# Kernel optimization log

Hardware: AMD Instinct MI355X
Metric: run time of the kernel (lower is better)

## Reference

```python
import jax, jax.numpy as jnp
import numpy as np

HEADS = 12
DIM_HEAD = 64
SCALE = DIM_HEAD ** -0.5

def setup_inputs() -> dict:
    key = jax.random.key(0)
    k1, k2, k3, k4 = jax.random.split(key, 4)
    dim, inner = 768, HEADS * DIM_HEAD
    x = jax.random.normal(k1, (4, 2048, dim), dtype=jnp.float32)
    w_qkv = jax.random.normal(k2, (dim, 3 * inner), dtype=jnp.float32) * (dim ** -0.5)
    w_out = jax.random.normal(k3, (inner, dim), dtype=jnp.float32) * (inner ** -0.5)
    b_out = jax.random.normal(k4, (dim,), dtype=jnp.float32) * 0.02
    return {"x": x, "w_qkv": w_qkv, "w_out": w_out, "b_out": b_out}

def reference(x, w_qkv, w_out, b_out):
    B, N, _ = x.shape
    qkv = jnp.einsum('bnd,de->bne', x, w_qkv)  # [B,N,3*inner]
    q, k, v = jnp.split(qkv, 3, axis=-1)
    # b n (h d) -> b h n d
    split_heads = lambda t: t.reshape(B, N, HEADS, DIM_HEAD).transpose(0, 2, 1, 3)
    q, k, v = split_heads(q), split_heads(k), split_heads(v)
    dots = jnp.einsum('bhnd,bhmd->bhnm', q, k) * SCALE  # [B,H,N,N]
    attn = jax.nn.softmax(dots, axis=-1)
    out = jnp.einsum('bhnm,bhmd->bhnd', attn, v)
    out = out.transpose(0, 2, 1, 3).reshape(B, N, HEADS * DIM_HEAD)  # b h n d -> b n (h d)
    return jnp.einsum('bne,ed->bnd', out, w_out) + b_out
```

## Files before the change

### kernel.cpp

```cpp
#include <hip/hip_runtime.h>
#include <stdint.h>

typedef unsigned short ushort_t;
typedef __attribute__((ext_vector_type(8))) short short8;
typedef __attribute__((ext_vector_type(4))) float f32x4;
typedef __attribute__((ext_vector_type(2))) uint32_t u32x2;

#define BATCH 4
#define SEQ 2048
#define DMODEL 768
#define NH 12
#define HD 64
#define QKV3 2304
#define NHEADS 48
#define SCALE_Q 0.18033688011112042f

__device__ __forceinline__ ushort_t f2bf(float f) {
    union { float f; uint32_t u; } v; v.f = f;
    uint32_t u = v.u;
    u += 0x7FFF + ((u >> 16) & 1);
    return (ushort_t)(u >> 16);
}

__device__ __forceinline__ uint32_t pack_bf16(float a, float b) {
#if __has_builtin(__builtin_amdgcn_cvt_pk_bf16_f32)
    typedef __attribute__((ext_vector_type(2))) __bf16 bf16x2;
    bf16x2 r = __builtin_amdgcn_cvt_pk_bf16_f32(a, b);
    return __builtin_bit_cast(uint32_t, r);
#else
    return ((uint32_t)f2bf(b) << 16) | (uint32_t)f2bf(a);
#endif
}

typedef __attribute__((address_space(1))) uint32_t as1_u32;
typedef __attribute__((address_space(3))) uint32_t as3_u32;
__device__ __forceinline__ void async16(void* lds, const void* gsrc) {
    __builtin_amdgcn_global_load_lds((as1_u32*)gsrc, (as3_u32*)lds, 16, 0, 0);
}

__device__ __forceinline__ void wait_vm_lgkm0() {
    __builtin_amdgcn_s_waitcnt(0x0070);
}
__device__ __forceinline__ void wait_vm4_lgkm0() {
    __builtin_amdgcn_s_waitcnt(0x0074);
}

__device__ __forceinline__ void swap32(uint32_t& a, uint32_t& b) {
    asm("v_permlane32_swap_b32 %0, %1" : "+v"(a), "+v"(b));
}
__device__ __forceinline__ void swap16(uint32_t& a, uint32_t& b) {
    asm("v_permlane16_swap_b32 %0, %1" : "+v"(a), "+v"(b));
}

__global__ __launch_bounds__(256) void cvt_bf16(
    const float* __restrict__ in, ushort_t* __restrict__ out) {
    int i = blockIdx.x * 256 + threadIdx.x;
    float4 v = *(const float4*)(in + (size_t)i * 4);
    ushort4 o; o.x = f2bf(v.x); o.y = f2bf(v.y); o.z = f2bf(v.z); o.w = f2bf(v.w);
    *(ushort4*)(out + (size_t)i * 4) = o;
}

__global__ __launch_bounds__(256) void transpose_f32_bf16(
    const float* __restrict__ in, ushort_t* __restrict__ out, int R, int C) {
    __shared__ ushort_t t[64][72];
    const int tid = threadIdx.x;
    const int r0 = blockIdx.y * 64, c0 = blockIdx.x * 64;
#pragma unroll
    for (int i = 0; i < 4; i++) {
        int idx = tid + i * 256;
        int row = idx >> 4, c4 = (idx & 15) * 4;
        float4 v = *(const float4*)(in + (size_t)(r0 + row) * C + c0 + c4);
        ushort4 o; o.x = f2bf(v.x); o.y = f2bf(v.y); o.z = f2bf(v.z); o.w = f2bf(v.w);
        *(ushort4*)&t[row][c4] = o;
    }
    __syncthreads();
#pragma unroll
    for (int i = 0; i < 2; i++) {
        int idx = tid + i * 256;
        int oc = idx >> 3, g8 = (idx & 7) * 8;
        ushort_t tmp[8];
#pragma unroll
        for (int e = 0; e < 8; e++) tmp[e] = t[g8 + e][oc];
        *(short8*)(out + (size_t)(c0 + oc) * R + r0 + g8) = *(const short8*)tmp;
    }
}

__global__ __launch_bounds__(256, 2) void gemm_qkv(
    const ushort_t* __restrict__ A, const ushort_t* __restrict__ B,
    ushort_t* __restrict__ qkv, ushort_t* __restrict__ vT) {
    __shared__ ushort_t As[2][128 * 64];
    __shared__ ushort_t Bs[2][128 * 64];

    const int tid = threadIdx.x;
    const int m0 = blockIdx.y * 128, n0 = blockIdx.x * 128;
    const int lane = tid & 63, w = tid >> 6;
    const int wm = w >> 1, wn = w & 1;
    const int l16 = lane & 15, quad = lane >> 4;

    f32x4 acc[4][4];
#pragma unroll
    for (int i = 0; i < 4; i++)
#pragma unroll
        for (int j = 0; j < 4; j++) acc[i][j] = (f32x4){0.f, 0.f, 0.f, 0.f};

    int srow[4], scol[4];
#pragma unroll
    for (int j = 0; j < 4; j++) {
        int s = j * 256 + tid;
        srow[j] = s >> 3;
        scol[j] = ((s & 7) ^ (srow[j] & 7)) * 8;
    }
    const int swz0 = (quad ^ (l16 & 7)) * 8;
    const int swz1 = ((4 + quad) ^ (l16 & 7)) * 8;

    auto stage = [&](int kt, int buf) {
#pragma unroll
        for (int j = 0; j < 4; j++) {
            async16(&As[buf][(j * 256 + w * 64) * 8],
                    A + (size_t)(m0 + srow[j]) * DMODEL + kt * 64 + scol[j]);
            async16(&Bs[buf][(j * 256 + w * 64) * 8],
                    B + (size_t)(n0 + srow[j]) * DMODEL + kt * 64 + scol[j]);
        }
    };

    stage(0, 0);
    const int NKT = DMODEL / 64;
    for (int t = 0; t < NKT; t++) {
        wait_vm_lgkm0();
        __builtin_amdgcn_s_barrier();
        if (t + 1 < NKT) stage(t + 1, (t + 1) & 1);

        const ushort_t* Asb = As[t & 1];
        const ushort_t* Bsb = Bs[t & 1];
        short8 a[4][2], b[4][2];
#pragma unroll
        for (int mi = 0; mi < 4; mi++) {
            int r = (wm * 64 + mi * 16 + l16) * 64;
            a[mi][0] = *(const short8*)&Asb[r + swz0];
            a[mi][1] = *(const short8*)&Asb[r + swz1];
        }
#pragma unroll
        for (int ni = 0; ni < 4; ni++) {
            int r = (wn * 64 + ni * 16 + l16) * 64;
            b[ni][0] = *(const short8*)&Bsb[r + swz0];
            b[ni][1] = *(const short8*)&Bsb[r + swz1];
        }
#pragma unroll
        for (int kk = 0; kk < 2; kk++)
#pragma unroll
            for (int mi = 0; mi < 4; mi++)
#pragma unroll
                for (int ni = 0; ni < 4; ni++)
                    acc[mi][ni] = __builtin_amdgcn_mfma_f32_16x16x32_bf16(
                        a[mi][kk], b[ni][kk], acc[mi][ni], 0, 0, 0);
    }

#pragma unroll
    for (int ni = 0; ni < 4; ni++) {
        int nbase = n0 + wn * 64 + ni * 16;
        int which = nbase / DMODEL;
        int rem = nbase - which * DMODEL;
        int h = rem >> 6;
        int d = (rem & 63) + l16;
        if (which == 2) {
#pragma unroll
            for (int mi = 0; mi < 4; mi++) {
                int mg = m0 + wm * 64 + mi * 16 + quad * 4;
                int b_ = mg >> 11, ns = mg & 2047;
                u32x2 pk = {pack_bf16(acc[mi][ni][0], acc[mi][ni][1]),
                            pack_bf16(acc[mi][ni][2], acc[mi][ni][3])};
                *(u32x2*)(vT + ((size_t)(b_ * NH + h) * HD + d) * SEQ + ns) = pk;
            }
        } else {
            float scale = (which == 0) ? SCALE_Q : 1.0f;
#pragma unroll
            for (int mi = 0; mi < 4; mi++) {
#pragma unroll
                for (int r = 0; r < 4; r++) {
                    int mg = m0 + wm * 64 + mi * 16 + quad * 4 + r;
                    int b_ = mg >> 11, ns = mg & 2047;
                    size_t dst = (((size_t)(which * BATCH + b_) * NH + h) * SEQ + ns) * HD + d;
                    qkv[dst] = f2bf(acc[mi][ni][r] * scale);
                }
            }
        }
    }
}

__global__ __launch_bounds__(256, 3) void attn(
    const ushort_t* __restrict__ qkv, const ushort_t* __restrict__ vT,
    ushort_t* __restrict__ ao) {
    __shared__ ushort_t smem[24576];

    const int tid = threadIdx.x;
    const int bid = blockIdx.x;
    const int i = bid >> 3;
    const int bh = (bid & 7) + 8 * (i % 6);
    const int qt = i / 6;
    const int lane = tid & 63, w = tid >> 6;
    const int l16 = lane & 15, quad = lane >> 4;
    const int qh7 = l16 & 7;

    const ushort_t* qh = qkv + (size_t)bh * (SEQ * HD);
    const ushort_t* kh = qkv + (size_t)(NHEADS + bh) * (SEQ * HD);
    const ushort_t* vh = vT + (size_t)bh * (HD * SEQ);

    short8 aq[2][2];
#pragma unroll
    for (int mi = 0; mi < 2; mi++)
#pragma unroll
        for (int kk = 0; kk < 2; kk++) {
            int row = qt * 128 + w * 32 + mi * 16 + l16;
            aq[mi][kk] = *(const short8*)(qh + (size_t)row * HD + kk * 32 + quad * 8);
        }

    short8 ones8;
#pragma unroll
    for (int j = 0; j < 8; j++) ones8[j] = (short)0x3F80;

    f32x4 acc_l[2];
    f32x4 O[4][2];
#pragma unroll
    for (int mi = 0; mi < 2; mi++) acc_l[mi] = (f32x4){0.f, 0.f, 0.f, 0.f};
#pragma unroll
    for (int nd = 0; nd < 4; nd++)
#pragma unroll
        for (int mi = 0; mi < 2; mi++) O[nd][mi] = (f32x4){0.f, 0.f, 0.f, 0.f};

    int srow[2], scol[2];
#pragma unroll
    for (int j = 0; j < 2; j++) {
        int s = j * 256 + tid;
        srow[j] = s >> 3;
        scol[j] = ((s & 7) ^ (srow[j] & 7)) * 8;
    }
    const int swz0 = (quad ^ qh7) * 8;
    const int swz1 = ((4 + quad) ^ qh7) * 8;

    auto stage = [&](int t, int buf) {
        int nb = buf * 8192, j1 = t * 64;
#pragma unroll
        for (int j = 0; j < 2; j++) {
            async16(&smem[nb + (j * 256 + w * 64) * 8],
                    kh + (size_t)(j1 + srow[j]) * HD + scol[j]);
            async16(&smem[nb + 4096 + (j * 256 + w * 64) * 8],
                    vh + (size_t)srow[j] * SEQ + j1 + scol[j]);
        }
    };

    auto compute = [&](const ushort_t* Ks) {
        const ushort_t* Vs = Ks + 4096;
#pragma unroll
        for (int p = 0; p < 2; p++) {
            uint32_t pkv[2][2][2];
#pragma unroll
            for (int sub = 0; sub < 2; sub++) {
                const int ni = p * 2 + sub;
                int r = (ni * 16 + l16) * 64;
                short8 ak0 = *(const short8*)&Ks[r + swz0];
                short8 ak1 = *(const short8*)&Ks[r + swz1];
#pragma unroll
                for (int mi = 0; mi < 2; mi++) {
                    f32x4 s = __builtin_amdgcn_mfma_f32_16x16x32_bf16(
                        ak0, aq[mi][0], (f32x4){0.f, 0.f, 0.f, 0.f}, 0, 0, 0);
                    s = __builtin_amdgcn_mfma_f32_16x16x32_bf16(
                        ak1, aq[mi][1], s, 0, 0, 0);
                    f32x4 pr;
#pragma unroll
                    for (int rr = 0; rr < 4; rr++)
                        pr[rr] = __builtin_amdgcn_exp2f(s[rr]);
                    pkv[sub][mi][0] = pack_bf16(pr[0], pr[1]);
                    pkv[sub][mi][1] = pack_bf16(pr[2], pr[3]);
                }
            }
            short8 bp32[2];
#pragma unroll
            for (int mi = 0; mi < 2; mi++) {
                uint32_t x0 = pkv[0][mi][0], y0 = pkv[1][mi][0];
                uint32_t x1 = pkv[0][mi][1], y1 = pkv[1][mi][1];
                swap32(x0, y0); swap16(x0, y0);
                swap32(x1, y1); swap16(x1, y1);
                union { short8 s; uint32_t u[4]; } bu;
                bu.u[0] = x0; bu.u[1] = x1; bu.u[2] = y0; bu.u[3] = y1;
                bp32[mi] = bu.s;
            }
            __builtin_amdgcn_s_setprio(1);
#pragma unroll
            for (int mi = 0; mi < 2; mi++)
                acc_l[mi] = __builtin_amdgcn_mfma_f32_16x16x32_bf16(
                    ones8, bp32[mi], acc_l[mi], 0, 0, 0);
#pragma unroll
            for (int nd = 0; nd < 4; nd++) {
                int vrow = nd * 16 + l16;
                short8 av = *(const short8*)&Vs[vrow * 64 +
                                                (((p * 4 + quad) ^ qh7) * 8)];
#pragma unroll
                for (int mi = 0; mi < 2; mi++)
                    O[nd][mi] = __builtin_amdgcn_mfma_f32_16x16x32_bf16(
                        av, bp32[mi], O[nd][mi], 0, 0, 0);
            }
            __builtin_amdgcn_s_setprio(0);
        }
    };

    stage(0, 0);
    stage(1, 1);

    const int NT = SEQ / 64;
    for (int t = 0; t < NT - 1; t++) {
        wait_vm4_lgkm0();
        __builtin_amdgcn_s_barrier();
        if (t + 2 < NT) stage(t + 2, (t + 2) % 3);
        compute(smem + (t % 3) * 8192);
    }
    wait_vm_lgkm0();
    __builtin_amdgcn_s_barrier();
    compute(smem + ((NT - 1) % 3) * 8192);

    float inv[2];
#pragma unroll
    for (int mi = 0; mi < 2; mi++)
        inv[mi] = __builtin_amdgcn_rcpf(acc_l[mi][0]);
    __syncthreads();
    ushort_t* Lt = smem;
#pragma unroll
    for (int mi = 0; mi < 2; mi++)
#pragma unroll
        for (int nd = 0; nd < 4; nd++) {
            int row = w * 32 + mi * 16 + l16;
            int col = nd * 16 + quad * 4;
            uint32_t d0 = pack_bf16(O[nd][mi][0] * inv[mi], O[nd][mi][1] * inv[mi]);
            uint32_t d1 = pack_bf16(O[nd][mi][2] * inv[mi], O[nd][mi][3] * inv[mi]);
            *(u32x2*)&Lt[row * 72 + col] = (u32x2){d0, d1};
        }
    __syncthreads();

    const int b_ = bh / NH, h = bh % NH;
#pragma unroll
    for (int i2 = 0; i2 < 4; i2++) {
        int idx = tid + i2 * 256;
        int row = idx >> 3, c8 = (idx & 7) * 8;
        short8 vv = *(const short8*)&Lt[row * 72 + c8];
        *(short8*)(ao + ((size_t)(b_ * SEQ + qt * 128 + row)) * DMODEL +
                   h * HD + c8) = vv;
    }
}

__global__ __launch_bounds__(256, 2) void gemm_out(
    const ushort_t* __restrict__ A, const ushort_t* __restrict__ B,
    const float* __restrict__ bias, float* __restrict__ out) {
    __shared__ ushort_t As[2][128 * 64];
    __shared__ ushort_t Bs[2][128 * 64];

    const int tid = threadIdx.x;
    const int m0 = blockIdx.y * 128, n0 = blockIdx.x * 128;
    const int lane = tid & 63, w = tid >> 6;
    const int wm = w >> 1, wn = w & 1;
    const int l16 = lane & 15, quad = lane >> 4;

    f32x4 acc[4][4];
#pragma unroll
    for (int i = 0; i < 4; i++)
#pragma unroll
        for (int j = 0; j < 4; j++) acc[i][j] = (f32x4){0.f, 0.f, 0.f, 0.f};

    int srow[4], scol[4];
#pragma unroll
    for (int j = 0; j < 4; j++) {
        int s = j * 256 + tid;
        srow[j] = s >> 3;
        scol[j] = ((s & 7) ^ (srow[j] & 7)) * 8;
    }
    const int swz0 = (quad ^ (l16 & 7)) * 8;
    const int swz1 = ((4 + quad) ^ (l16 & 7)) * 8;

    auto stage = [&](int kt, int buf) {
#pragma unroll
        for (int j = 0; j < 4; j++) {
            async16(&As[buf][(j * 256 + w * 64) * 8],
                    A + (size_t)(m0 + srow[j]) * DMODEL + kt * 64 + scol[j]);
            async16(&Bs[buf][(j * 256 + w * 64) * 8],
                    B + (size_t)(n0 + srow[j]) * DMODEL + kt * 64 + scol[j]);
        }
    };

    stage(0, 0);
    const int NKT = DMODEL / 64;
    for (int t = 0; t < NKT; t++) {
        wait_vm_lgkm0();
        __builtin_amdgcn_s_barrier();
        if (t + 1 < NKT) stage(t + 1, (t + 1) & 1);

        const ushort_t* Asb = As[t & 1];
        const ushort_t* Bsb = Bs[t & 1];
        short8 a[4][2], b[4][2];
#pragma unroll
        for (int mi = 0; mi < 4; mi++) {
            int r = (wm * 64 + mi * 16 + l16) * 64;
            a[mi][0] = *(const short8*)&Asb[r + swz0];
            a[mi][1] = *(const short8*)&Asb[r + swz1];
        }
#pragma unroll
        for (int ni = 0; ni < 4; ni++) {
            int r = (wn * 64 + ni * 16 + l16) * 64;
            b[ni][0] = *(const short8*)&Bsb[r + swz0];
            b[ni][1] = *(const short8*)&Bsb[r + swz1];
        }
#pragma unroll
        for (int kk = 0; kk < 2; kk++)
#pragma unroll
            for (int mi = 0; mi < 4; mi++)
#pragma unroll
                for (int ni = 0; ni < 4; ni++)
                    acc[mi][ni] = __builtin_amdgcn_mfma_f32_16x16x32_bf16(
                        a[mi][kk], b[ni][kk], acc[mi][ni], 0, 0, 0);
    }

#pragma unroll
    for (int ni = 0; ni < 4; ni++) {
        int ng = n0 + wn * 64 + ni * 16 + l16;
        float bv = bias[ng];
#pragma unroll
        for (int mi = 0; mi < 4; mi++) {
#pragma unroll
            for (int r = 0; r < 4; r++) {
                int mg = m0 + wm * 64 + mi * 16 + quad * 4 + r;
                out[(size_t)mg * DMODEL + ng] = acc[mi][ni][r] + bv;
            }
        }
    }
}

extern "C" void kernel_launch(void* const* d_in, const int* in_sizes, int n_in,
                              void* d_out, int out_size, void* d_ws, size_t ws_size,
                              hipStream_t stream) {
    const float* x     = (const float*)d_in[0];
    const float* w_qkv = (const float*)d_in[1];
    const float* w_out = (const float*)d_in[2];
    const float* b_out = (const float*)d_in[3];
    float* out = (float*)d_out;

    ushort_t* xb  = (ushort_t*)d_ws;
    ushort_t* wqT = xb  + (size_t)8192 * 768;
    ushort_t* woT = wqT + (size_t)QKV3 * 768;
    ushort_t* qkv = woT + (size_t)768 * 768;
    ushort_t* vT  = qkv + (size_t)3 * NHEADS * SEQ * HD;
    ushort_t* ao  = vT  + (size_t)NHEADS * HD * SEQ;

    cvt_bf16<<<dim3((8192 * 768) / 4 / 256), 256, 0, stream>>>(x, xb);
    transpose_f32_bf16<<<dim3(QKV3 / 64, DMODEL / 64), 256, 0, stream>>>(
        w_qkv, wqT, DMODEL, QKV3);
    transpose_f32_bf16<<<dim3(DMODEL / 64, DMODEL / 64), 256, 0, stream>>>(
        w_out, woT, DMODEL, DMODEL);

    gemm_qkv<<<dim3(QKV3 / 128, (BATCH * SEQ) / 128), 256, 0, stream>>>(
        xb, wqT, qkv, vT);

    attn<<<dim3(NHEADS * (SEQ / 128)), 256, 0, stream>>>(qkv, vT, ao);

    gemm_out<<<dim3(DMODEL / 128, (BATCH * SEQ) / 128), 256, 0, stream>>>(
        ao, woT, b_out, out);
}
```

Baseline: 214.9 us.

## Prefetch two K-tiles ahead in GEMMs and merge prep kernels into one launch

The three preprocessing kernels (x conversion to bf16 and two weight transposes) are merged into a single launch that picks its job by block index, removing two kernel launches. Both GEMMs now stage tiles t and t+1 up front. Each iteration waits only until the current tile has landed (vmcnt 8), reads its fragments into registers, then takes a second barrier and issues the load for tile t+2 into the buffer just freed, so global loads overlap two iterations of MFMA work. The cost is an extra barrier per K step, and correctness relies on the hand-written waitcnt values.

```diff
diff --git a/kernel.cpp b/kernel.cpp
--- a/kernel.cpp
+++ b/kernel.cpp
@@ -44,6 +44,12 @@
 __device__ __forceinline__ void wait_vm4_lgkm0() {
     __builtin_amdgcn_s_waitcnt(0x0074);
 }
+__device__ __forceinline__ void wait_vm8_lgkm0() {
+    __builtin_amdgcn_s_waitcnt(0x0078);
+}
+__device__ __forceinline__ void wait_lgkm0_only() {
+    __builtin_amdgcn_s_waitcnt(0xC07F);
+}
 
 __device__ __forceinline__ void swap32(uint32_t& a, uint32_t& b) {
     asm("v_permlane32_swap_b32 %0, %1" : "+v"(a), "+v"(b));
@@ -52,19 +58,9 @@
     asm("v_permlane16_swap_b32 %0, %1" : "+v"(a), "+v"(b));
 }
 
-__global__ __launch_bounds__(256) void cvt_bf16(
-    const float* __restrict__ in, ushort_t* __restrict__ out) {
-    int i = blockIdx.x * 256 + threadIdx.x;
-    float4 v = *(const float4*)(in + (size_t)i * 4);
-    ushort4 o; o.x = f2bf(v.x); o.y = f2bf(v.y); o.z = f2bf(v.z); o.w = f2bf(v.w);
-    *(ushort4*)(out + (size_t)i * 4) = o;
-}
-
-__global__ __launch_bounds__(256) void transpose_f32_bf16(
-    const float* __restrict__ in, ushort_t* __restrict__ out, int R, int C) {
-    __shared__ ushort_t t[64][72];
-    const int tid = threadIdx.x;
-    const int r0 = blockIdx.y * 64, c0 = blockIdx.x * 64;
+__device__ __forceinline__ void transpose_body(
+    const float* __restrict__ in, ushort_t* __restrict__ out,
+    int R, int C, int r0, int c0, int tid, ushort_t (*t)[72]) {
 #pragma unroll
     for (int i = 0; i < 4; i++) {
         int idx = tid + i * 256;
@@ -85,6 +81,28 @@
     }
 }
 
+__global__ __launch_bounds__(256) void prep(
+    const float* __restrict__ x, ushort_t* __restrict__ xb,
+    const float* __restrict__ w_qkv, ushort_t* __restrict__ wqT,
+    const float* __restrict__ w_out, ushort_t* __restrict__ woT) {
+    __shared__ ushort_t t[64][72];
+    const int b = blockIdx.x, tid = threadIdx.x;
+    if (b < 6144) {
+        size_t i = (size_t)b * 256 + tid;
+        float4 v = *(const float4*)(x + i * 4);
+        ushort4 o; o.x = f2bf(v.x); o.y = f2bf(v.y); o.z = f2bf(v.z); o.w = f2bf(v.w);
+        *(ushort4*)(xb + i * 4) = o;
+    } else if (b < 6144 + 432) {
+        int tb = b - 6144;
+        int bx = tb % 36, by = tb / 36;
+        transpose_body(w_qkv, wqT, DMODEL, QKV3, by * 64, bx * 64, tid, t);
+    } else {
+        int tb = b - 6576;
+        int bx = tb % 12, by = tb / 12;
+        transpose_body(w_out, woT, DMODEL, DMODEL, by * 64, bx * 64, tid, t);
+    }
+}
+
 __global__ __launch_bounds__(256, 2) void gemm_qkv(
     const ushort_t* __restrict__ A, const ushort_t* __restrict__ B,
     ushort_t* __restrict__ qkv, ushort_t* __restrict__ vT) {
@@ -124,11 +142,12 @@
     };
 
     stage(0, 0);
+    stage(1, 1);
     const int NKT = DMODEL / 64;
     for (int t = 0; t < NKT; t++) {
-        wait_vm_lgkm0();
+        if (t < NKT - 1) wait_vm8_lgkm0();
+        else             wait_vm_lgkm0();
         __builtin_amdgcn_s_barrier();
-        if (t + 1 < NKT) stage(t + 1, (t + 1) & 1);
 
         const ushort_t* Asb = As[t & 1];
         const ushort_t* Bsb = Bs[t & 1];
@@ -145,6 +164,11 @@
             b[ni][0] = *(const short8*)&Bsb[r + swz0];
             b[ni][1] = *(const short8*)&Bsb[r + swz1];
         }
+        wait_lgkm0_only();
+        __builtin_amdgcn_sched_barrier(0);
+        __builtin_amdgcn_s_barrier();
+        if (t + 2 < NKT) stage(t + 2, t & 1);
+
 #pragma unroll
         for (int kk = 0; kk < 2; kk++)
 #pragma unroll
@@ -385,11 +409,12 @@
     };
 
     stage(0, 0);
+    stage(1, 1);
     const int NKT = DMODEL / 64;
     for (int t = 0; t < NKT; t++) {
-        wait_vm_lgkm0();
+        if (t < NKT - 1) wait_vm8_lgkm0();
+        else             wait_vm_lgkm0();
         __builtin_amdgcn_s_barrier();
-        if (t + 1 < NKT) stage(t + 1, (t + 1) & 1);
 
         const ushort_t* Asb = As[t & 1];
         const ushort_t* Bsb = Bs[t & 1];
@@ -406,6 +431,11 @@
             b[ni][0] = *(const short8*)&Bsb[r + swz0];
             b[ni][1] = *(const short8*)&Bsb[r + swz1];
         }
+        wait_lgkm0_only();
+        __builtin_amdgcn_sched_barrier(0);
+        __builtin_amdgcn_s_barrier();
+        if (t + 2 < NKT) stage(t + 2, t & 1);
+
 #pragma unroll
         for (int kk = 0; kk < 2; kk++)
 #pragma unroll
@@ -447,11 +477,7 @@
     ushort_t* vT  = qkv + (size_t)3 * NHEADS * SEQ * HD;
     ushort_t* ao  = vT  + (size_t)NHEADS * HD * SEQ;
 
-    cvt_bf16<<<dim3((8192 * 768) / 4 / 256), 256, 0, stream>>>(x, xb);
-    transpose_f32_bf16<<<dim3(QKV3 / 64, DMODEL / 64), 256, 0, stream>>>(
-        w_qkv, wqT, DMODEL, QKV3);
-    transpose_f32_bf16<<<dim3(DMODEL / 64, DMODEL / 64), 256, 0, stream>>>(
-        w_out, woT, DMODEL, DMODEL);
+    prep<<<dim3(6720), 256, 0, stream>>>(x, xb, w_qkv, wqT, w_out, woT);
 
     gemm_qkv<<<dim3(QKV3 / 128, (BATCH * SEQ) / 128), 256, 0, stream>>>(
         xb, wqT, qkv, vT);
```

Result: no change. 214.6 us (-0.2%).
